# Optimization experiments

Hardware: AMD Instinct MI355X
Metric: run time of the kernel (lower is better)

## Reference

```python
import jax, jax.numpy as jnp
import numpy as np

N, T, D, P, NB = 32768, 128, 32, 16, 15


def setup_inputs() -> dict:
    key = jax.random.key(0)
    ks = jax.random.split(key, 8)
    S = jax.random.normal(ks[0], (N, T, 1), dtype=jnp.float32)
    L_dyn = jax.random.normal(ks[1], (N, T, D), dtype=jnp.float32)
    C_static = jax.random.normal(ks[2], (N, P), dtype=jnp.float32)
    Y = jax.random.randint(ks[3], (N, T, 1), 0, 2).astype(jnp.float32)
    mask = jnp.ones((N, T), dtype=jnp.float32)
    return {
        "S": S, "L_dyn": L_dyn, "C_static": C_static, "Y": Y, "mask": mask,
        "psi": jnp.array([0.5], jnp.float32),
        "gamma_A": jnp.array([0.1], jnp.float32),
        "w_gamma_dyn": 0.05 * jax.random.normal(ks[4], (D,), dtype=jnp.float32),
        "w_gamma_static": 0.05 * jax.random.normal(ks[5], (P,), dtype=jnp.float32),
        "log_sigma_Z": jnp.array([-0.5], jnp.float32),
        "beta_0": jnp.array([-4.0], jnp.float32),
        "beta_Z": jnp.array([0.3], jnp.float32),
        "beta_bins": jnp.zeros((NB,), jnp.float32),
        "w_beta_dyn": 0.1 * jax.random.normal(ks[6], (D,), dtype=jnp.float32),
        "w_beta_static": 0.1 * jax.random.normal(ks[7], (P,), dtype=jnp.float32),
        "beta_time": jnp.array([0.03], jnp.float32),
    }


def reference(S, L_dyn, C_static, Y, mask, psi, gamma_A, w_gamma_dyn,
              w_gamma_static, log_sigma_Z, beta_0, beta_Z, beta_bins,
              w_beta_dyn, w_beta_static, beta_time):
    n, t_len = S.shape[0], S.shape[1]
    nb = beta_bins.shape[0]
    edges = jnp.linspace(-2.5, 2.5, nb + 1).astype(S.dtype)
    # torch.bucketize(s, edges[1:-1]) (right=False) == searchsorted side='left'
    idx = jnp.clip(jnp.searchsorted(edges[1:-1], S[..., 0], side='left'), 0, nb - 1)
    bin_eff = beta_bins[idx][..., None]            # (N,T,1) == (A_bin * beta_bins).sum(-1)
    sigma_sq = jnp.exp(log_sigma_Z)[0] ** 2        # sigma_Z^2
    gd = L_dyn @ w_gamma_dyn[:, None]              # (N,T,1) gamma_dyn(L)
    bd = L_dyn @ w_beta_dyn[:, None]               # (N,T,1) beta_dyn(L)
    gs = (C_static @ w_gamma_static)[:, None]      # (N,1) gamma_static(C)
    bs = (C_static @ w_beta_static)[:, None]       # (N,1) beta_static(C)
    tt = jnp.arange(t_len, dtype=S.dtype) / 30.0   # beta_time * (t/30)

    xs = (
        jnp.swapaxes(S, 0, 1),        # (T,N,1)
        jnp.swapaxes(gd, 0, 1),
        jnp.swapaxes(bd, 0, 1),
        jnp.swapaxes(bin_eff, 0, 1),
        jnp.swapaxes(Y, 0, 1),
        mask.T[:, :, None],           # (T,N,1)
        tt,
    )
    psi_s, gA, bZ, b0, bT = psi[0], gamma_A[0], beta_Z[0], beta_0[0], beta_time[0]

    def step(carry, x):
        Z_mean, Z_var, ll = carry
        A_t, gd_t, bd_t, be_t, Y_t, m_t, t_s = x
        # latent transition prior
        Z_pred_mean = psi_s * Z_mean + gA * A_t + gd_t + gs
        Z_pred_var = psi_s ** 2 * Z_var + sigma_sq
        # outcome probability
        logit = b0 + bZ * Z_pred_mean + be_t + bd_t + bs + bT * t_s
        prob = jax.nn.sigmoid(jnp.clip(logit, -20.0, 20.0))
        # approximate Kalman (Laplace) update from Y
        grad = (Y_t - prob) * bZ * m_t
        hess = bZ ** 2 * prob * (1.0 - prob) * m_t + 1e-6
        Z_post_var = 1.0 / (1.0 / (Z_pred_var + 1e-8) + hess)
        Z_post_mean = Z_pred_mean + Z_post_var * grad
        ll_t = ((Y_t * jnp.log(prob + 1e-10)
                 + (1.0 - Y_t) * jnp.log(1.0 - prob + 1e-10)) * m_t).sum()
        return (Z_post_mean, Z_post_var, ll + ll_t), (Z_post_mean, Z_post_var)

    init = (jnp.zeros((n, 1), S.dtype), jnp.ones((n, 1), S.dtype),
            jnp.zeros((), S.dtype))
    (_, _, ll), (Zf, Zv) = jax.lax.scan(step, init, xs)
    return jnp.swapaxes(Zf, 0, 1), jnp.swapaxes(Zv, 0, 1), ll
```

## Files before the change

### kernel.cpp

```cpp
#include <hip/hip_runtime.h>

#define T_LEN 128
#define NB_BINS 15
#define SPB 16

__global__ __launch_bounds__(256) void k_all(
    const float*  __restrict__ S,
    const float*  __restrict__ Y,
    const float*  __restrict__ M,
    const float4* __restrict__ L4,
    const float4* __restrict__ C4,
    const float4* __restrict__ wgs4,
    const float4* __restrict__ wbs4,
    const float4* __restrict__ wgd4,
    const float4* __restrict__ wbd4,
    const float*  __restrict__ p_psi,
    const float*  __restrict__ p_gA,
    const float*  __restrict__ p_lsz,
    const float*  __restrict__ p_b0,
    const float*  __restrict__ p_bZ,
    const float*  __restrict__ p_bbins,
    const float*  __restrict__ p_bT,
    float4* __restrict__ Zf4,
    float4* __restrict__ Zv4,
    float*  __restrict__ ll_out)
{
    __shared__ float4 tile[T_LEN][SPB + 1];
    __shared__ float sgs[SPB], sbs[SPB];
    __shared__ float sbins[NB_BINS];

    const int tid = threadIdx.x;
    const int n0  = blockIdx.x * SPB;

    if (tid < NB_BINS) sbins[tid] = p_bbins[tid];
    if (tid < SPB) {
        float gs = 0.0f, bs = 0.0f;
        #pragma unroll
        for (int i = 0; i < 4; ++i) {
            float4 c  = C4[(n0 + tid) * 4 + i];
            float4 wg = wgs4[i];
            float4 wb = wbs4[i];
            gs += c.x * wg.x + c.y * wg.y + c.z * wg.z + c.w * wg.w;
            bs += c.x * wb.x + c.y * wb.y + c.z * wb.z + c.w * wb.w;
        }
        sgs[tid] = gs; sbs[tid] = bs;
    }
    __syncthreads();

    const float gA   = p_gA[0];
    const float b0   = p_b0[0];
    const float bT30 = p_bT[0] * (1.0f / 30.0f);

    const int lane8 = tid & 7;
    const int gid   = tid >> 3;
    const float4 wg = wgd4[lane8];
    const float4 wb = wbd4[lane8];
    const size_t rowbase = (size_t)n0 * T_LEN;

    float4 v = L4[(rowbase + gid) * 8 + lane8];
    for (int it = 0; it < 64; ++it) {
        const int    lrow = it * 32 + gid;
        const size_t row  = rowbase + lrow;

        float4 vn = v;
        if (it + 1 < 64) vn = L4[(row + 32) * 8 + lane8];

        float s_v = 0.0f, y_v = 0.0f, m_v = 0.0f;
        if (lane8 == 0) { s_v = S[row]; y_v = Y[row]; m_v = M[row]; }

        float g = v.x * wg.x + v.y * wg.y + v.z * wg.z + v.w * wg.w;
        float b = v.x * wb.x + v.y * wb.y + v.z * wb.z + v.w * wb.w;
        #pragma unroll
        for (int off = 1; off < 8; off <<= 1) {
            g += __shfl_xor(g, off, 64);
            b += __shfl_xor(b, off, 64);
        }

        if (lane8 == 0) {
            const int nl = lrow >> 7;
            const int t  = lrow & 127;
            int cnt = (int)fmaxf(0.0f, fminf(14.0f,
                          ceilf(fmaf(s_v, 3.0f, 7.5f)) - 1.0f));
            const float a = gA * s_v + g + sgs[nl];
            const float c = b0 + sbins[cnt] + b + sbs[nl] + bT30 * (float)t;
            tile[t][nl] = make_float4(a, c, y_v, m_v);
        }
        v = vn;
    }
    __syncthreads();

    float ll = 0.0f;
    if (tid < SPB) {
        const float psi  = p_psi[0];
        const float e    = __expf(p_lsz[0]);
        const float sig2 = e * e;
        const float bZ   = p_bZ[0];
        const float psi2 = psi * psi;
        const float bZ2  = bZ * bZ;

        float zm = 0.0f, zvv = 1.0f;
        const int    nl = tid;
        const size_t ob = (size_t)(n0 + nl) * 32;

        for (int cnk = 0; cnk < 16; ++cnk) {
            float pm[8], pv[8];
            #pragma unroll
            for (int j = 0; j < 8; ++j) {
                const float4 pk = tile[cnk * 8 + j][nl];
                const float zpm = fmaf(psi, zm, pk.x);
                const float zpv = fmaf(psi2, zvv, sig2);
                float logit = fmaf(bZ, zpm, pk.y);
                logit = fminf(fmaxf(logit, -20.0f), 20.0f);
                const float prob = __builtin_amdgcn_rcpf(1.0f + __expf(-logit));
                const float grad = (pk.z - prob) * bZ * pk.w;
                const float hess = fmaf(bZ2 * prob * (1.0f - prob), pk.w, 1e-6f);
                const float pvv  = __builtin_amdgcn_rcpf(
                                     __builtin_amdgcn_rcpf(zpv + 1e-8f) + hess);
                const float pmm  = fmaf(pvv, grad, zpm);
                ll += (pk.z * __logf(prob + 1e-10f)
                     + (1.0f - pk.z) * __logf(1.0f - prob + 1e-10f)) * pk.w;
                zm = pmm; zvv = pvv; pm[j] = pmm; pv[j] = pvv;
            }
            Zf4[ob + cnk * 2]     = make_float4(pm[0], pm[1], pm[2], pm[3]);
            Zf4[ob + cnk * 2 + 1] = make_float4(pm[4], pm[5], pm[6], pm[7]);
            Zv4[ob + cnk * 2]     = make_float4(pv[0], pv[1], pv[2], pv[3]);
            Zv4[ob + cnk * 2 + 1] = make_float4(pv[4], pv[5], pv[6], pv[7]);
        }
    }

    #pragma unroll
    for (int off = 1; off < 64; off <<= 1) ll += __shfl_xor(ll, off, 64);
    if (tid == 0) atomicAdd(ll_out, ll);
}

extern "C" void kernel_launch(void* const* d_in, const int* in_sizes, int n_in,
                              void* d_out, int out_size, void* d_ws, size_t ws_size,
                              hipStream_t stream) {
    const float* S     = (const float*)d_in[0];
    const float* L     = (const float*)d_in[1];
    const float* C     = (const float*)d_in[2];
    const float* Y     = (const float*)d_in[3];
    const float* M     = (const float*)d_in[4];
    const float* psi   = (const float*)d_in[5];
    const float* gA    = (const float*)d_in[6];
    const float* wgd   = (const float*)d_in[7];
    const float* wgs   = (const float*)d_in[8];
    const float* lsz   = (const float*)d_in[9];
    const float* b0    = (const float*)d_in[10];
    const float* bZ    = (const float*)d_in[11];
    const float* bbins = (const float*)d_in[12];
    const float* wbd   = (const float*)d_in[13];
    const float* wbs   = (const float*)d_in[14];
    const float* bT    = (const float*)d_in[15];

    const int NT    = in_sizes[0];
    const int n_seq = NT / T_LEN;

    float* zf = (float*)d_out;
    float* zv = zf + NT;
    float* ll = zf + 2 * (size_t)NT;

    hipMemsetAsync((void*)ll, 0, sizeof(float), stream);

    k_all<<<n_seq / SPB, 256, 0, stream>>>(
        S, Y, M,
        reinterpret_cast<const float4*>(L),
        reinterpret_cast<const float4*>(C),
        reinterpret_cast<const float4*>(wgs),
        reinterpret_cast<const float4*>(wbs),
        reinterpret_cast<const float4*>(wgd),
        reinterpret_cast<const float4*>(wbd),
        psi, gA, lsz, b0, bZ, bbins, bT,
        reinterpret_cast<float4*>(zf),
        reinterpret_cast<float4*>(zv),
        ll);
}
```

Baseline: 193.7 us.

## Split time axis into four passes with carried Kalman state and redundant per-lane scan

Replaces the single kernel, where only 16 threads per block ran the serial scan, with four launches that each cover a 32-step time slab. The latent mean and variance are carried between launches through a workspace buffer. In each pass every one of 32 lanes per sequence runs the full slab recurrence on its own and keeps only the output for its own time step, so the output stores are coalesced. The aim is to remove the idle-thread serial tail and the strided float4 stores. In exchange it adds launch overhead and carry traffic, and does 32x redundant recurrence arithmetic with an unrolled loop.

```diff
diff --git a/kernel.cpp b/kernel.cpp
--- a/kernel.cpp
+++ b/kernel.cpp
@@ -2,12 +2,13 @@
 
 #define T_LEN 128
 #define NB_BINS 15
-#define SPB 16
+#define TSLAB 32
+#define NPASS 4
 
-__global__ __launch_bounds__(256) void k_all(
+__global__ __launch_bounds__(1024) void k_pass(
     const float*  __restrict__ S,
     const float*  __restrict__ Y,
-    const float*  __restrict__ M,
+    const float*  __restrict__ Mm,
     const float4* __restrict__ L4,
     const float4* __restrict__ C4,
     const float4* __restrict__ wgs4,
@@ -21,116 +22,129 @@
     const float*  __restrict__ p_bZ,
     const float*  __restrict__ p_bbins,
     const float*  __restrict__ p_bT,
-    float4* __restrict__ Zf4,
-    float4* __restrict__ Zv4,
-    float*  __restrict__ ll_out)
+    float2* __restrict__ carry,
+    float*  __restrict__ zf,
+    float*  __restrict__ zvo,
+    float*  __restrict__ ll_out,
+    int pass)
 {
-    __shared__ float4 tile[T_LEN][SPB + 1];
-    __shared__ float sgs[SPB], sbs[SPB];
-    __shared__ float sbins[NB_BINS];
+    __shared__ float  ldsG[16][2][TSLAB];
+    __shared__ float  ldsB[16][2][TSLAB];
+    __shared__ float4 tile[16][2][TSLAB];
+    __shared__ float  ldsLL[16];
+    __shared__ float  sbins[NB_BINS];
 
-    const int tid = threadIdx.x;
-    const int n0  = blockIdx.x * SPB;
+    const int tid  = threadIdx.x;
+    if (tid < NB_BINS) sbins[tid] = p_bbins[tid];
 
-    if (tid < NB_BINS) sbins[tid] = p_bbins[tid];
-    if (tid < SPB) {
-        float gs = 0.0f, bs = 0.0f;
-        #pragma unroll
-        for (int i = 0; i < 4; ++i) {
-            float4 c  = C4[(n0 + tid) * 4 + i];
-            float4 wg = wgs4[i];
-            float4 wb = wbs4[i];
-            gs += c.x * wg.x + c.y * wg.y + c.z * wg.z + c.w * wg.w;
-            bs += c.x * wb.x + c.y * wb.y + c.z * wb.z + c.w * wb.w;
-        }
-        sgs[tid] = gs; sbs[tid] = bs;
+    const int w    = tid >> 6;
+    const int k    = tid & 63;
+    const int half = k >> 5;
+    const int kk   = k & 31;
+
+    const int n = blockIdx.x * 32 + w * 2 + half;
+
+    const size_t cb = (size_t)n * (T_LEN * 8) + (size_t)pass * (TSLAB * 8);
+    float4 Lb0 = L4[cb + 0*32 + kk], Lb1 = L4[cb + 1*32 + kk];
+    float4 Lb2 = L4[cb + 2*32 + kk], Lb3 = L4[cb + 3*32 + kk];
+    float4 Lb4 = L4[cb + 4*32 + kk], Lb5 = L4[cb + 5*32 + kk];
+    float4 Lb6 = L4[cb + 6*32 + kk], Lb7 = L4[cb + 7*32 + kk];
+
+    const int sb  = n * T_LEN + pass * TSLAB;
+    const float s_v = S[sb + kk];
+    const float y_v = Y[sb + kk];
+    const float m_v = Mm[sb + kk];
+
+    const float psi  = p_psi[0];
+    const float gA   = p_gA[0];
+    const float e    = __expf(p_lsz[0]);
+    const float sig2 = e * e;
+    const float b0   = p_b0[0];
+    const float bZ   = p_bZ[0];
+    const float bT30 = p_bT[0] * (1.0f / 30.0f);
+    const float psi2 = psi * psi;
+    const float bZ2  = bZ * bZ;
+
+    float gs, bs;
+    {
+        const int q = k & 3;
+        const float4 c  = C4[n * 4 + q];
+        const float4 wgq = wgs4[q];
+        const float4 wbq = wbs4[q];
+        gs = c.x*wgq.x + c.y*wgq.y + c.z*wgq.z + c.w*wgq.w;
+        bs = c.x*wbq.x + c.y*wbq.y + c.z*wbq.z + c.w*wbq.w;
+        gs += __shfl_xor(gs, 1, 64); gs += __shfl_xor(gs, 2, 64);
+        bs += __shfl_xor(bs, 1, 64); bs += __shfl_xor(bs, 2, 64);
+    }
+
+    {
+        const float4 wgq = wgd4[k & 7];
+        const float4 wbq = wbd4[k & 7];
+#define DOT(i, Lb) do {                                                       \
+        float g = Lb.x*wgq.x + Lb.y*wgq.y + Lb.z*wgq.z + Lb.w*wgq.w;          \
+        float b = Lb.x*wbq.x + Lb.y*wbq.y + Lb.z*wbq.z + Lb.w*wbq.w;          \
+        g += __shfl_xor(g, 1, 64); g += __shfl_xor(g, 2, 64);                 \
+        g += __shfl_xor(g, 4, 64);                                            \
+        b += __shfl_xor(b, 1, 64); b += __shfl_xor(b, 2, 64);                 \
+        b += __shfl_xor(b, 4, 64);                                            \
+        if ((k & 7) == 0) {                                                   \
+            const int t = (i) * 4 + (kk >> 3);                                \
+            ldsG[w][half][t] = g; ldsB[w][half][t] = b;                       \
+        }                                                                     \
+    } while (0)
+        DOT(0, Lb0); DOT(1, Lb1); DOT(2, Lb2); DOT(3, Lb3);
+        DOT(4, Lb4); DOT(5, Lb5); DOT(6, Lb6); DOT(7, Lb7);
+#undef DOT
     }
     __syncthreads();
 
-    const float gA   = p_gA[0];
-    const float b0   = p_b0[0];
-    const float bT30 = p_bT[0] * (1.0f / 30.0f);
-
-    const int lane8 = tid & 7;
-    const int gid   = tid >> 3;
-    const float4 wg = wgd4[lane8];
-    const float4 wb = wbd4[lane8];
-    const size_t rowbase = (size_t)n0 * T_LEN;
-
-    float4 v = L4[(rowbase + gid) * 8 + lane8];
-    for (int it = 0; it < 64; ++it) {
-        const int    lrow = it * 32 + gid;
-        const size_t row  = rowbase + lrow;
-
-        float4 vn = v;
-        if (it + 1 < 64) vn = L4[(row + 32) * 8 + lane8];
-
-        float s_v = 0.0f, y_v = 0.0f, m_v = 0.0f;
-        if (lane8 == 0) { s_v = S[row]; y_v = Y[row]; m_v = M[row]; }
-
-        float g = v.x * wg.x + v.y * wg.y + v.z * wg.z + v.w * wg.w;
-        float b = v.x * wb.x + v.y * wb.y + v.z * wb.z + v.w * wb.w;
-        #pragma unroll
-        for (int off = 1; off < 8; off <<= 1) {
-            g += __shfl_xor(g, off, 64);
-            b += __shfl_xor(b, off, 64);
-        }
-
-        if (lane8 == 0) {
-            const int nl = lrow >> 7;
-            const int t  = lrow & 127;
-            int cnt = (int)fmaxf(0.0f, fminf(14.0f,
-                          ceilf(fmaf(s_v, 3.0f, 7.5f)) - 1.0f));
-            const float a = gA * s_v + g + sgs[nl];
-            const float c = b0 + sbins[cnt] + b + sbs[nl] + bT30 * (float)t;
-            tile[t][nl] = make_float4(a, c, y_v, m_v);
-        }
-        v = vn;
+    {
+        int cnt = (int)fmaxf(0.0f, fminf(14.0f,
+                      ceilf(fmaf(s_v, 3.0f, 7.5f)) - 1.0f));
+        const float a = gA * s_v + ldsG[w][half][kk] + gs;
+        const float c = b0 + sbins[cnt] + ldsB[w][half][kk] + bs
+                      + bT30 * (float)(pass * TSLAB + kk);
+        tile[w][half][kk] = make_float4(a, c, y_v, m_v);
     }
     __syncthreads();
 
-    float ll = 0.0f;
-    if (tid < SPB) {
-        const float psi  = p_psi[0];
-        const float e    = __expf(p_lsz[0]);
-        const float sig2 = e * e;
-        const float bZ   = p_bZ[0];
-        const float psi2 = psi * psi;
-        const float bZ2  = bZ * bZ;
+    float zm, zvv;
+    if (pass == 0) { zm = 0.0f; zvv = 1.0f; }
+    else           { const float2 c2 = carry[n]; zm = c2.x; zvv = c2.y; }
 
-        float zm = 0.0f, zvv = 1.0f;
-        const int    nl = tid;
-        const size_t ob = (size_t)(n0 + nl) * 32;
-
-        for (int cnk = 0; cnk < 16; ++cnk) {
-            float pm[8], pv[8];
-            #pragma unroll
-            for (int j = 0; j < 8; ++j) {
-                const float4 pk = tile[cnk * 8 + j][nl];
-                const float zpm = fmaf(psi, zm, pk.x);
-                const float zpv = fmaf(psi2, zvv, sig2);
-                float logit = fmaf(bZ, zpm, pk.y);
-                logit = fminf(fmaxf(logit, -20.0f), 20.0f);
-                const float prob = __builtin_amdgcn_rcpf(1.0f + __expf(-logit));
-                const float grad = (pk.z - prob) * bZ * pk.w;
-                const float hess = fmaf(bZ2 * prob * (1.0f - prob), pk.w, 1e-6f);
-                const float pvv  = __builtin_amdgcn_rcpf(
-                                     __builtin_amdgcn_rcpf(zpv + 1e-8f) + hess);
-                const float pmm  = fmaf(pvv, grad, zpm);
-                ll += (pk.z * __logf(prob + 1e-10f)
-                     + (1.0f - pk.z) * __logf(1.0f - prob + 1e-10f)) * pk.w;
-                zm = pmm; zvv = pvv; pm[j] = pmm; pv[j] = pvv;
-            }
-            Zf4[ob + cnk * 2]     = make_float4(pm[0], pm[1], pm[2], pm[3]);
-            Zf4[ob + cnk * 2 + 1] = make_float4(pm[4], pm[5], pm[6], pm[7]);
-            Zv4[ob + cnk * 2]     = make_float4(pv[0], pv[1], pv[2], pv[3]);
-            Zv4[ob + cnk * 2 + 1] = make_float4(pv[4], pv[5], pv[6], pv[7]);
-        }
+    float ll = 0.0f, pmk = 0.0f, pvk = 0.0f;
+    #pragma unroll
+    for (int t = 0; t < TSLAB; ++t) {
+        const float4 pk = tile[w][half][t];
+        const float zpm = fmaf(psi, zm, pk.x);
+        const float zpv = fmaf(psi2, zvv, sig2);
+        float logit = fmaf(bZ, zpm, pk.y);
+        logit = fminf(fmaxf(logit, -20.0f), 20.0f);
+        const float prob = __builtin_amdgcn_rcpf(1.0f + __expf(-logit));
+        const float grad = (pk.z - prob) * bZ * pk.w;
+        const float hess = fmaf(bZ2 * prob * (1.0f - prob), pk.w, 1e-6f);
+        const float pvv  = __builtin_amdgcn_rcpf(
+                             __builtin_amdgcn_rcpf(zpv + 1e-8f) + hess);
+        const float pmm  = fmaf(pvv, grad, zpm);
+        ll += (pk.z * __logf(prob + 1e-10f)
+             + (1.0f - pk.z) * __logf(1.0f - prob + 1e-10f)) * pk.w;
+        zm = pmm; zvv = pvv;
+        if (t == kk) { pmk = pmm; pvk = pvv; }
     }
 
-    #pragma unroll
-    for (int off = 1; off < 64; off <<= 1) ll += __shfl_xor(ll, off, 64);
-    if (tid == 0) atomicAdd(ll_out, ll);
+    if (kk == 0) carry[n] = make_float2(zm, zvv);
+    zf [sb + kk] = pmk;
+    zvo[sb + kk] = pvk;
+
+    float llw = ll + __shfl_xor(ll, 32, 64);
+    if (k == 0) ldsLL[w] = llw;
+    __syncthreads();
+    if (tid == 0) {
+        float t = 0.0f;
+        #pragma unroll
+        for (int i = 0; i < 16; ++i) t += ldsLL[i];
+        atomicAdd(ll_out, t);
+    }
 }
 
 extern "C" void kernel_launch(void* const* d_in, const int* in_sizes, int n_in,
@@ -160,18 +174,21 @@
     float* zv = zf + NT;
     float* ll = zf + 2 * (size_t)NT;
 
+    float2* carry = (float2*)d_ws;
+
     hipMemsetAsync((void*)ll, 0, sizeof(float), stream);
 
-    k_all<<<n_seq / SPB, 256, 0, stream>>>(
-        S, Y, M,
-        reinterpret_cast<const float4*>(L),
-        reinterpret_cast<const float4*>(C),
-        reinterpret_cast<const float4*>(wgs),
-        reinterpret_cast<const float4*>(wbs),
-        reinterpret_cast<const float4*>(wgd),
-        reinterpret_cast<const float4*>(wbd),
-        psi, gA, lsz, b0, bZ, bbins, bT,
-        reinterpret_cast<float4*>(zf),
-        reinterpret_cast<float4*>(zv),
-        ll);
+    const int blocks = n_seq / 32;
+    for (int p = 0; p < NPASS; ++p) {
+        k_pass<<<blocks, 1024, 0, stream>>>(
+            S, Y, M,
+            reinterpret_cast<const float4*>(L),
+            reinterpret_cast<const float4*>(C),
+            reinterpret_cast<const float4*>(wgs),
+            reinterpret_cast<const float4*>(wbs),
+            reinterpret_cast<const float4*>(wgd),
+            reinterpret_cast<const float4*>(wbd),
+            psi, gA, lsz, b0, bZ, bbins, bT,
+            carry, zf, zv, ll, p);
+    }
 }
```

New measurement: 742.3 us. 283% more time.
